# Kernel tuning notes

Measured on AMD Instinct MI355X. Metric: run time of the kernel, lower is better.

## Reference

```python
import jax, jax.numpy as jnp
import numpy as np

B, S, D, H = 2, 2048, 1024, 16
DK = D // H
NEG = -1e9


def setup_inputs() -> dict:
    key = jax.random.key(0)
    ks = jax.random.split(key, 12)
    inp = {
        "query": jax.random.normal(ks[0], (B, S, D), jnp.float32),
        "key": jax.random.normal(ks[1], (B, S, D), jnp.float32),
        "value": jax.random.normal(ks[2], (B, S, D), jnp.float32),
        "mask": jax.random.randint(ks[3], (B, S), 0, 2, jnp.int32),
    }
    # 4 linears (q, k, v, out), each d_model x d_model with bias.
    scale = 1.0 / np.sqrt(D)
    for i, name in enumerate(["wq", "wk", "wv", "wo"]):
        inp[name] = jax.random.uniform(ks[4 + i], (D, D), jnp.float32, -scale, scale)
        inp["b" + name[1]] = jax.random.uniform(ks[8 + i], (D,), jnp.float32, -scale, scale)
    return inp


def _split_heads(x):  # [B,S,D] -> [B,H,S,DK]
    return x.reshape(B, S, H, DK).transpose(0, 2, 1, 3)


def reference(query, key, value, mask, wq, bq, wk, bk, wv, bv, wo, bo):
    q = _split_heads(query @ wq.T + bq)
    k = _split_heads(key @ wk.T + bk)
    v = _split_heads(value @ wv.T + bv)
    scores = jnp.einsum("bhqd,bhkd->bhqk", q, k) / jnp.sqrt(jnp.float32(DK))
    # mask: [B,S] -> [B,1,1,S]; masked_fill where mask == 0
    m = mask[:, None, None, :]
    scores = jnp.where(m == 0, NEG, scores)
    attn = jax.nn.softmax(scores, axis=-1)  # dropout p=0 (eval) -> identity
    x = jnp.einsum("bhqk,bhkd->bhqd", attn, v)
    x = x.transpose(0, 2, 1, 3).reshape(B, S, D)
    return x @ wo.T + bo
```

## Files before the change

kernel.cpp:

```cpp
#include <hip/hip_runtime.h>


typedef _Float16 f16;
typedef _Float16 f16x8 __attribute__((ext_vector_type(8)));
typedef _Float16 f16x4 __attribute__((ext_vector_type(4)));
typedef __fp16 fp16x2r __attribute__((ext_vector_type(2)));
typedef float f32x4 __attribute__((ext_vector_type(4)));

#define MFMA_F16(a, b, c) __builtin_amdgcn_mfma_f32_16x16x32_f16((a), (b), (c), 0, 0, 0)
#define L2E 1.44269504088896340736f

__device__ __forceinline__ void gld16(const void* g, void* l) {
    __builtin_amdgcn_global_load_lds(
        (__attribute__((address_space(1))) void*)(g),
        (__attribute__((address_space(3))) void*)(l), 16, 0, 0);
}

__global__ __launch_bounds__(256) void cvt_kernel(
    const float* __restrict__ q, const float* __restrict__ k,
    const float* __restrict__ v,
    const float* __restrict__ wq, const float* __restrict__ wk,
    const float* __restrict__ wv, const float* __restrict__ wo,
    f16* __restrict__ oq, f16* __restrict__ ok, f16* __restrict__ ov,
    f16* __restrict__ owq, f16* __restrict__ owk, f16* __restrict__ owv,
    f16* __restrict__ owo)
{
    const int z = blockIdx.y;
    const float* src;
    f16* dst;
    int n;
    switch (z) {
        case 0: src = q;  dst = oq;  n = 4194304; break;
        case 1: src = k;  dst = ok;  n = 4194304; break;
        case 2: src = v;  dst = ov;  n = 4194304; break;
        case 3: src = wq; dst = owq; n = 1048576; break;
        case 4: src = wk; dst = owk; n = 1048576; break;
        case 5: src = wv; dst = owv; n = 1048576; break;
        default: src = wo; dst = owo; n = 1048576; break;
    }
    int idx = (blockIdx.x * 256 + threadIdx.x) * 8;
    if (idx >= n) return;
    float4 a = *(const float4*)(src + idx);
    float4 b = *(const float4*)(src + idx + 4);
    f16x8 h = { (f16)a.x, (f16)a.y, (f16)a.z, (f16)a.w,
                (f16)b.x, (f16)b.y, (f16)b.z, (f16)b.w };
    *(f16x8*)(dst + idx) = h;
}

__global__ __launch_bounds__(256) void proj_qkv_kernel(
    const f16* __restrict__ xq, const f16* __restrict__ xk,
    const f16* __restrict__ xv,
    const f16* __restrict__ wqh, const f16* __restrict__ wkh,
    const f16* __restrict__ wvh,
    const float* __restrict__ bq, const float* __restrict__ bk,
    const float* __restrict__ bv,
    f16* __restrict__ qh, f16* __restrict__ kh, f16* __restrict__ vt)
{
    const int z = blockIdx.z;
    const f16* X = (z == 0) ? xq : (z == 1) ? xk : xv;
    const f16* W = (z == 0) ? wqh : (z == 1) ? wkh : wvh;
    const float* bias = (z == 0) ? bq : (z == 1) ? bk : bv;
    const f16* P0 = (z < 2) ? W : X;
    const f16* P1 = (z < 2) ? X : W;

    __shared__ __align__(16) f16 smem[16384];
    f16* As = smem;
    f16* Bs = smem + 8192;
    f16* L  = smem;

    const int t = threadIdx.x;
    const int wave = t >> 6, lane = t & 63, quad = lane >> 4, l15 = lane & 15;
    const int m_base = (wave >> 1) * 64, n_base = (wave & 1) * 64;
    const int blockM = (z < 2) ? blockIdx.y * 128 : blockIdx.x * 128;
    const int blockN = (z < 2) ? blockIdx.x * 128 : blockIdx.y * 128;

    const int srow = lane >> 3;
    const int sblk = (lane & 7) ^ srow;

    f32x4 acc[4][4];
#pragma unroll
    for (int mt = 0; mt < 4; mt++)
#pragma unroll
        for (int nt = 0; nt < 4; nt++)
            acc[mt][nt] = (f32x4){0.f, 0.f, 0.f, 0.f};

    for (int k0 = 0; k0 < 1024; k0 += 64) {
        __syncthreads();
#pragma unroll
        for (int j = 0; j < 4; j++) {
            int r0 = wave * 32 + j * 8;
            gld16(&P0[(size_t)(blockM + r0 + srow) * 1024 + k0 + sblk * 8],
                  &As[r0 * 64]);
            gld16(&P1[(size_t)(blockN + r0 + srow) * 1024 + k0 + sblk * 8],
                  &Bs[r0 * 64]);
        }
        __syncthreads();

#pragma unroll
        for (int c = 0; c < 2; c++) {
            f16x8 af[4], bf[4];
#pragma unroll
            for (int mt = 0; mt < 4; mt++)
                af[mt] = *(const f16x8*)(&As[(m_base + mt * 16 + l15) * 64 +
                                             (((c * 4 + quad) ^ (l15 & 7)) << 3)]);
#pragma unroll
            for (int nt = 0; nt < 4; nt++)
                bf[nt] = *(const f16x8*)(&Bs[(n_base + nt * 16 + l15) * 64 +
                                             (((c * 4 + quad) ^ (l15 & 7)) << 3)]);
#pragma unroll
            for (int mt = 0; mt < 4; mt++)
#pragma unroll
                for (int nt = 0; nt < 4; nt++)
                    acc[mt][nt] = MFMA_F16(af[mt], bf[nt], acc[mt][nt]);
        }
    }

    if (z < 2) {
        f16* o = (z == 0) ? qh : kh;
        const float scale = (z == 0) ? 0.125f * L2E : 1.0f;
        float4 b4[4];
#pragma unroll
        for (int mt = 0; mt < 4; mt++)
            b4[mt] = *(const float4*)(&bias[blockM + m_base + mt * 16 + quad * 4]);

#pragma unroll
        for (int half = 0; half < 2; half++) {
            __syncthreads();
            if ((wave & 1) == half) {
#pragma unroll
                for (int mt = 0; mt < 4; mt++)
#pragma unroll
                    for (int nt = 0; nt < 4; nt++) {
                        f16x4 pk = {
                            (f16)((acc[mt][nt][0] + b4[mt].x) * scale),
                            (f16)((acc[mt][nt][1] + b4[mt].y) * scale),
                            (f16)((acc[mt][nt][2] + b4[mt].z) * scale),
                            (f16)((acc[mt][nt][3] + b4[mt].w) * scale) };
                        *(f16x4*)(&L[(nt * 16 + l15) * 136 +
                                     m_base + mt * 16 + quad * 4]) = pk;
                    }
            }
            __syncthreads();
#pragma unroll
            for (int pass = 0; pass < 4; pass++) {
                int unit = pass * 32 + (t >> 3);
                int hh = unit >> 6, s_loc = unit & 63;
                f16x8 vv = *(const f16x8*)(&L[s_loc * 136 + hh * 64 + (t & 7) * 8]);
                int s_glob = blockN + half * 64 + s_loc;
                int b = s_glob >> 11, s = s_glob & 2047;
                int h_glob = (blockM >> 6) + hh;
                *(f16x8*)(&o[(((size_t)(b * 16 + h_glob) * 2048 + s) << 6) +
                             (t & 7) * 8]) = vv;
            }
        }
    } else {
        float bv_[4];
#pragma unroll
        for (int nt = 0; nt < 4; nt++)
            bv_[nt] = bias[blockN + n_base + nt * 16 + l15];

#pragma unroll
        for (int half = 0; half < 2; half++) {
            __syncthreads();
            if ((wave & 1) == half) {
#pragma unroll
                for (int mt = 0; mt < 4; mt++)
#pragma unroll
                    for (int nt = 0; nt < 4; nt++) {
                        f16x4 pk = { (f16)(acc[mt][nt][0] + bv_[nt]),
                                     (f16)(acc[mt][nt][1] + bv_[nt]),
                                     (f16)(acc[mt][nt][2] + bv_[nt]),
                                     (f16)(acc[mt][nt][3] + bv_[nt]) };
                        *(f16x4*)(&L[(nt * 16 + l15) * 136 +
                                     m_base + mt * 16 + quad * 4]) = pk;
                    }
            }
            __syncthreads();
#pragma unroll
            for (int pass = 0; pass < 4; pass++) {
                int f_loc = pass * 16 + (t >> 4);
                int tt = t & 15;
                int bb = (tt >= 8) ? 64 : 0;
                int o  = (tt & 7) * 8;
                int p  = (o >> 5) & 1;
                int c  = (o >> 3) & 3;
                int g1 = bb + p * 32 + c * 4;
                const f16* Lrow = &L[f_loc * 136];
                f16x4 lo = *(const f16x4*)(&Lrow[g1]);
                f16x4 hi = *(const f16x4*)(&Lrow[g1 + 16]);
                f16x8 vv = __builtin_shufflevector(lo, hi, 0, 1, 2, 3, 4, 5, 6, 7);
                int feat = blockN + half * 64 + f_loc;
                int hh = feat >> 6, dk = feat & 63;
                int b = blockM >> 11;
                int s0 = (blockM & 2047) + bb + o;
                *(f16x8*)(&vt[((size_t)((b * 16 + hh) * 64 + dk) << 11) + s0]) = vv;
            }
        }
    }
}

__device__ __forceinline__ void flash_stage2(
    const f16* kbase, const f16* vbase, int key0,
    f16* Kb, f16* Vb, int wg, int srow8, int sblk)
{
#pragma unroll
    for (int p = 0; p < 2; p++) {
        int r0 = wg * 16 + p * 8;
        int row = r0 + srow8;
        gld16(&kbase[(size_t)(key0 + row) * 64 + sblk * 8], &Kb[r0 * 64]);
        gld16(&vbase[(size_t)row * 2048 + key0 + sblk * 8], &Vb[r0 * 64]);
    }
}

__device__ __forceinline__ void flash_phase2(
    const f16* Kbuf, const f16* Vbuf, const float* bias_all, int key0,
    const f16x8 (&qf)[2][2], int quad, int l15,
    f32x4 (&O)[2][4], f32x4 (&lacc)[2])
{
    const int sw = l15 & 7;
    f32x4 sc[2][4];
#pragma unroll
    for (int nt = 0; nt < 4; nt++) {
        const f16* krow = &Kbuf[(nt * 16 + l15) * 64];
        f16x8 kf0 = *(const f16x8*)(&krow[(quad ^ sw) << 3]);
        f16x8 kf1 = *(const f16x8*)(&krow[((quad + 4) ^ sw) << 3]);
        float4 b4 = *(const float4*)(&bias_all[key0 + nt * 16 + quad * 4]);
#pragma unroll
        for (int cb = 0; cb < 2; cb++) {
            f32x4 z4 = (f32x4){b4.x, b4.y, b4.z, b4.w};
            z4 = MFMA_F16(kf0, qf[cb][0], z4);
            sc[cb][nt] = MFMA_F16(kf1, qf[cb][1], z4);
        }
    }
    const f16x8 ones8 = {(f16)1.f, (f16)1.f, (f16)1.f, (f16)1.f,
                         (f16)1.f, (f16)1.f, (f16)1.f, (f16)1.f};
    union P8u { f16x8 v8; fp16x2r h[4]; };
    P8u pp[2][2];
#pragma unroll
    for (int cb = 0; cb < 2; cb++) {
#pragma unroll
        for (int nt = 0; nt < 4; nt++) {
            float p0 = __builtin_amdgcn_exp2f(sc[cb][nt][0]);
            float p1 = __builtin_amdgcn_exp2f(sc[cb][nt][1]);
            float p2 = __builtin_amdgcn_exp2f(sc[cb][nt][2]);
            float p3 = __builtin_amdgcn_exp2f(sc[cb][nt][3]);
            pp[cb][nt >> 1].h[(nt & 1) * 2 + 0] = __builtin_amdgcn_cvt_pkrtz(p0, p1);
            pp[cb][nt >> 1].h[(nt & 1) * 2 + 1] = __builtin_amdgcn_cvt_pkrtz(p2, p3);
        }
        lacc[cb] = MFMA_F16(ones8, pp[cb][0].v8, lacc[cb]);
        lacc[cb] = MFMA_F16(ones8, pp[cb][1].v8, lacc[cb]);
    }
#pragma unroll
    for (int nto = 0; nto < 4; nto++) {
        const f16* vrow = &Vbuf[(nto * 16 + l15) * 64];
        f16x8 va = *(const f16x8*)(&vrow[(quad ^ sw) << 3]);
        f16x8 vb = *(const f16x8*)(&vrow[((4 + quad) ^ sw) << 3]);
#pragma unroll
        for (int cb = 0; cb < 2; cb++) {
            O[cb][nto] = MFMA_F16(va, pp[cb][0].v8, O[cb][nto]);
            O[cb][nto] = MFMA_F16(vb, pp[cb][1].v8, O[cb][nto]);
        }
    }
}

__global__
__attribute__((amdgpu_flat_work_group_size(512, 512)))
__attribute__((amdgpu_waves_per_eu(4, 4)))
void flash_kernel(
    const f16* __restrict__ qh, const f16* __restrict__ kh,
    const f16* __restrict__ vt, const int* __restrict__ mask,
    f16* __restrict__ ctx)
{
    __shared__ __align__(16) f16 KV[8 * 4096];
    __shared__ float bias_all[2048];

    const int t = threadIdx.x;
    const int wave = t >> 6, lane = t & 63, quad = lane >> 4, l15 = lane & 15;
    const int group = wave >> 2, wg = wave & 3;
    const int bh = blockIdx.x;
    const int b = bh >> 4, h = bh & 15;
    const int q0 = blockIdx.y * 128;

    const f16* qbase = qh + (size_t)bh * (2048 * 64);
    const f16* kbase = kh + (size_t)bh * (2048 * 64);
    const f16* vbase = vt + (size_t)bh * (64 * 2048);

    f16* K0 = &KV[((0 * 2 + group) * 2 + 0) * 4096];
    f16* V0 = &KV[((0 * 2 + group) * 2 + 1) * 4096];
    f16* K1 = &KV[((1 * 2 + group) * 2 + 0) * 4096];
    f16* V1 = &KV[((1 * 2 + group) * 2 + 1) * 4096];

#pragma unroll
    for (int j = 0; j < 4; j++) {
        int i = j * 512 + t;
        bias_all[i] = (mask[b * 2048 + i] == 0) ? -1.0e9f : 0.0f;
    }

    f16x8 qf[2][2];
#pragma unroll
    for (int cb = 0; cb < 2; cb++) {
        int qrow = q0 + wg * 32 + cb * 16 + l15;
        qf[cb][0] = *(const f16x8*)(&qbase[qrow * 64 + quad * 8]);
        qf[cb][1] = *(const f16x8*)(&qbase[qrow * 64 + 32 + quad * 8]);
    }

    f32x4 O[2][4];
#pragma unroll
    for (int cb = 0; cb < 2; cb++)
#pragma unroll
        for (int n = 0; n < 4; n++) O[cb][n] = (f32x4){0.f, 0.f, 0.f, 0.f};
    f32x4 lacc[2] = {(f32x4){0.f, 0.f, 0.f, 0.f}, (f32x4){0.f, 0.f, 0.f, 0.f}};

    const int srow8 = lane >> 3;
    const int sblk = (lane & 7) ^ srow8;

    flash_stage2(kbase, vbase, group * 64, K0, V0, wg, srow8, sblk);

    for (int k2 = 0; k2 < 16; k2 += 2) {
        __syncthreads();
        flash_stage2(kbase, vbase, (k2 + 1) * 128 + group * 64, K1, V1,
                     wg, srow8, sblk);
        flash_phase2(K0, V0, bias_all, k2 * 128 + group * 64,
                     qf, quad, l15, O, lacc);
        __syncthreads();
        if (k2 < 14)
            flash_stage2(kbase, vbase, (k2 + 2) * 128 + group * 64, K0, V0,
                         wg, srow8, sblk);
        flash_phase2(K1, V1, bias_all, (k2 + 1) * 128 + group * 64,
                     qf, quad, l15, O, lacc);
    }

    __syncthreads();
    float* Red = (float*)KV;
    const int t4 = wg * 64 + lane;
    if (group == 1) {
#pragma unroll
        for (int cb = 0; cb < 2; cb++) {
#pragma unroll
            for (int nto = 0; nto < 4; nto++)
                *(f32x4*)(&Red[(cb * 4 + nto) * 1024 + t4 * 4]) = O[cb][nto];
            Red[8 * 1024 + cb * 256 + t4] = lacc[cb][0];
        }
    }
    __syncthreads();
    if (group == 0) {
#pragma unroll
        for (int cb = 0; cb < 2; cb++) {
            const float l2 = Red[8 * 1024 + cb * 256 + t4];
            const float inv_l = 1.0f / (lacc[cb][0] + l2);
            int qrow = q0 + wg * 32 + cb * 16 + l15;
#pragma unroll
            for (int nto = 0; nto < 4; nto++) {
                f32x4 o2 = *(const f32x4*)(&Red[(cb * 4 + nto) * 1024 + t4 * 4]);
                f16x4 pk = { (f16)((O[cb][nto][0] + o2[0]) * inv_l),
                             (f16)((O[cb][nto][1] + o2[1]) * inv_l),
                             (f16)((O[cb][nto][2] + o2[2]) * inv_l),
                             (f16)((O[cb][nto][3] + o2[3]) * inv_l) };
                *(f16x4*)(&ctx[(size_t)(b * 2048 + qrow) * 1024 + h * 64 +
                               nto * 16 + quad * 4]) = pk;
            }
        }
    }
}

__global__ __launch_bounds__(256) void proj_out_kernel(
    const f16* __restrict__ ctx, const f16* __restrict__ woh,
    const float* __restrict__ bo, float* __restrict__ out)
{
    __shared__ __align__(16) f16 As[2][128 * 64];
    __shared__ __align__(16) f16 Bs[2][64 * 64];

    const int t = threadIdx.x;
    const int wave = t >> 6, lane = t & 63, quad = lane >> 4, l15 = lane & 15;
    const int m_base = (wave >> 1) * 64, n_base = (wave & 1) * 32;
    const int blockM = blockIdx.x * 128;
    const int blockN = blockIdx.y * 64;

    const int srow = lane >> 3;
    const int sblk = (lane & 7) ^ srow;

    f32x4 acc[4][2];
#pragma unroll
    for (int mt = 0; mt < 4; mt++)
#pragma unroll
        for (int nt = 0; nt < 2; nt++)
            acc[mt][nt] = (f32x4){0.f, 0.f, 0.f, 0.f};

#pragma unroll
    for (int j = 0; j < 4; j++) {
        int r0 = wave * 32 + j * 8;
        gld16(&ctx[(size_t)(blockM + r0 + srow) * 1024 + sblk * 8],
              &As[0][r0 * 64]);
    }
#pragma unroll
    for (int j = 0; j < 2; j++) {
        int r0 = wave * 16 + j * 8;
        gld16(&woh[(size_t)(blockN + r0 + srow) * 1024 + sblk * 8],
              &Bs[0][r0 * 64]);
    }

    for (int ki = 0; ki < 16; ki++) {
        const int cur = ki & 1;
        __syncthreads();

        if (ki < 15) {
            const int k0n = (ki + 1) * 64;
#pragma unroll
            for (int j = 0; j < 4; j++) {
                int r0 = wave * 32 + j * 8;
                gld16(&ctx[(size_t)(blockM + r0 + srow) * 1024 + k0n + sblk * 8],
                      &As[cur ^ 1][r0 * 64]);
            }
#pragma unroll
            for (int j = 0; j < 2; j++) {
                int r0 = wave * 16 + j * 8;
                gld16(&woh[(size_t)(blockN + r0 + srow) * 1024 + k0n + sblk * 8],
                      &Bs[cur ^ 1][r0 * 64]);
            }
        }

#pragma unroll
        for (int c = 0; c < 2; c++) {
            f16x8 af[4], bf[2];
#pragma unroll
            for (int mt = 0; mt < 4; mt++)
                af[mt] = *(const f16x8*)(&As[cur][(m_base + mt * 16 + l15) * 64 +
                                              (((c * 4 + quad) ^ (l15 & 7)) << 3)]);
#pragma unroll
            for (int nt = 0; nt < 2; nt++)
                bf[nt] = *(const f16x8*)(&Bs[cur][(n_base + nt * 16 + l15) * 64 +
                                              (((c * 4 + quad) ^ (l15 & 7)) << 3)]);
#pragma unroll
            for (int mt = 0; mt < 4; mt++)
#pragma unroll
                for (int nt = 0; nt < 2; nt++)
                    acc[mt][nt] = MFMA_F16(af[mt], bf[nt], acc[mt][nt]);
        }
    }

    float bo_[2];
#pragma unroll
    for (int nt = 0; nt < 2; nt++)
        bo_[nt] = bo[blockN + n_base + nt * 16 + l15];

#pragma unroll
    for (int mt = 0; mt < 4; mt++) {
        int row0 = blockM + m_base + mt * 16 + quad * 4;
#pragma unroll
        for (int nt = 0; nt < 2; nt++) {
            int col_g = blockN + n_base + nt * 16 + l15;
#pragma unroll
            for (int i = 0; i < 4; i++)
                out[(size_t)(row0 + i) * 1024 + col_g] = acc[mt][nt][i] + bo_[nt];
        }
    }
}

extern "C" void kernel_launch(void* const* d_in, const int* in_sizes, int n_in,
                              void* d_out, int out_size, void* d_ws, size_t ws_size,
                              hipStream_t stream) {
    const float* query = (const float*)d_in[0];
    const float* key_  = (const float*)d_in[1];
    const float* value = (const float*)d_in[2];
    const int*   mask  = (const int*)d_in[3];
    const float* wq = (const float*)d_in[4];
    const float* bq = (const float*)d_in[5];
    const float* wk = (const float*)d_in[6];
    const float* bk = (const float*)d_in[7];
    const float* wv = (const float*)d_in[8];
    const float* bv = (const float*)d_in[9];
    const float* wo = (const float*)d_in[10];
    const float* bo = (const float*)d_in[11];
    float* out = (float*)d_out;

    f16* xq  = (f16*)d_ws;
    f16* xk  = xq  + 4194304;
    f16* xv  = xk  + 4194304;
    f16* wqh = xv  + 4194304;
    f16* wkh = wqh + 1048576;
    f16* wvh = wkh + 1048576;
    f16* woh = wvh + 1048576;
    f16* qh  = woh + 1048576;
    f16* kh  = qh  + 4194304;
    f16* vt  = kh  + 4194304;
    f16* ctx = xq;

    cvt_kernel<<<dim3(2048, 7), 256, 0, stream>>>(
        query, key_, value, wq, wk, wv, wo, xq, xk, xv, wqh, wkh, wvh, woh);
    proj_qkv_kernel<<<dim3(32, 8, 3), 256, 0, stream>>>(
        xq, xk, xv, wqh, wkh, wvh, bq, bk, bv, qh, kh, vt);
    flash_kernel<<<dim3(32, 16), 512, 0, stream>>>(qh, kh, vt, mask, ctx);
    proj_out_kernel<<<dim3(32, 16), 256, 0, stream>>>(ctx, woh, bo, out);
}
```

Baseline: 212.7 us.

## Triple-buffer projection GEMMs with K=32 stages and explicit vmcnt waits

Both the QKV projection and output projection GEMMs move from single/double-buffered K=64 tiles to a three-stage ring of K=32 tiles. Each stage is loaded directly into LDS with global_load_lds, and the loop waits through manual s_waitcnt vmcnt counts plus raw s_barrier, so loads for two steps ahead overlap MFMA work. The LDS XOR swizzle is reworked for 32-wide rows. This raises LDS use and depends on hand-counted outstanding-load accounting, which could race if the counts are wrong.

New measurement: 209.2 us. No clear change (-1.6%).

```diff
diff --git a/kernel.cpp b/kernel.cpp
--- a/kernel.cpp
+++ b/kernel.cpp
@@ -47,6 +47,21 @@
     *(f16x8*)(dst + idx) = h;
 }
 
+__device__ __forceinline__ void stage_qkv(
+    const f16* __restrict__ P0, const f16* __restrict__ P1,
+    int blockM, int blockN, int k0, f16* Ad, f16* Bd,
+    int wave, int srow2, int schunk)
+{
+#pragma unroll
+    for (int p = 0; p < 2; p++) {
+        int r0 = wave * 32 + p * 16;
+        gld16(&P0[(size_t)(blockM + r0 + srow2) * 1024 + k0 + schunk * 8],
+              &Ad[r0 * 32]);
+        gld16(&P1[(size_t)(blockN + r0 + srow2) * 1024 + k0 + schunk * 8],
+              &Bd[r0 * 32]);
+    }
+}
+
 __global__ __launch_bounds__(256) void proj_qkv_kernel(
     const f16* __restrict__ xq, const f16* __restrict__ xk,
     const f16* __restrict__ xv,
@@ -63,10 +78,8 @@
     const f16* P0 = (z < 2) ? W : X;
     const f16* P1 = (z < 2) ? X : W;
 
-    __shared__ __align__(16) f16 smem[16384];
-    f16* As = smem;
-    f16* Bs = smem + 8192;
-    f16* L  = smem;
+    __shared__ __align__(16) f16 smem[24576];
+    f16* L = smem;
 
     const int t = threadIdx.x;
     const int wave = t >> 6, lane = t & 63, quad = lane >> 4, l15 = lane & 15;
@@ -74,8 +87,8 @@
     const int blockM = (z < 2) ? blockIdx.y * 128 : blockIdx.x * 128;
     const int blockN = (z < 2) ? blockIdx.x * 128 : blockIdx.y * 128;
 
-    const int srow = lane >> 3;
-    const int sblk = (lane & 7) ^ srow;
+    const int srow2 = lane >> 2;
+    const int schunk = (lane & 3) ^ (srow2 & 3);
 
     f32x4 acc[4][4];
 #pragma unroll
@@ -84,35 +97,41 @@
         for (int nt = 0; nt < 4; nt++)
             acc[mt][nt] = (f32x4){0.f, 0.f, 0.f, 0.f};
 
-    for (int k0 = 0; k0 < 1024; k0 += 64) {
-        __syncthreads();
-#pragma unroll
-        for (int j = 0; j < 4; j++) {
-            int r0 = wave * 32 + j * 8;
-            gld16(&P0[(size_t)(blockM + r0 + srow) * 1024 + k0 + sblk * 8],
-                  &As[r0 * 64]);
-            gld16(&P1[(size_t)(blockN + r0 + srow) * 1024 + k0 + sblk * 8],
-                  &Bs[r0 * 64]);
-        }
-        __syncthreads();
-
-#pragma unroll
-        for (int c = 0; c < 2; c++) {
-            f16x8 af[4], bf[4];
-#pragma unroll
-            for (int mt = 0; mt < 4; mt++)
-                af[mt] = *(const f16x8*)(&As[(m_base + mt * 16 + l15) * 64 +
-                                             (((c * 4 + quad) ^ (l15 & 7)) << 3)]);
+    f16 *Ac = smem,          *An = smem + 4096,  *Af = smem + 8192;
+    f16 *Bc = smem + 12288,  *Bn = smem + 16384, *Bf = smem + 20480;
+
+    stage_qkv(P0, P1, blockM, blockN, 0,  Ac, Bc, wave, srow2, schunk);
+    stage_qkv(P0, P1, blockM, blockN, 32, An, Bn, wave, srow2, schunk);
+    asm volatile("s_waitcnt vmcnt(4)" ::: "memory");
+
+    for (int ki = 0; ki < 32; ki++) {
+        __builtin_amdgcn_s_barrier();
+        __builtin_amdgcn_sched_barrier(0);
+        if (ki < 30)
+            stage_qkv(P0, P1, blockM, blockN, (ki + 2) * 32, Af, Bf,
+                      wave, srow2, schunk);
+
+        f16x8 af[4], bf[4];
+#pragma unroll
+        for (int mt = 0; mt < 4; mt++)
+            af[mt] = *(const f16x8*)(&Ac[(m_base + mt * 16 + l15) * 32 +
+                                         ((quad ^ (l15 & 3)) << 3)]);
+#pragma unroll
+        for (int nt = 0; nt < 4; nt++)
+            bf[nt] = *(const f16x8*)(&Bc[(n_base + nt * 16 + l15) * 32 +
+                                         ((quad ^ (l15 & 3)) << 3)]);
+#pragma unroll
+        for (int mt = 0; mt < 4; mt++)
 #pragma unroll
             for (int nt = 0; nt < 4; nt++)
-                bf[nt] = *(const f16x8*)(&Bs[(n_base + nt * 16 + l15) * 64 +
-                                             (((c * 4 + quad) ^ (l15 & 7)) << 3)]);
-#pragma unroll
-            for (int mt = 0; mt < 4; mt++)
-#pragma unroll
-                for (int nt = 0; nt < 4; nt++)
-                    acc[mt][nt] = MFMA_F16(af[mt], bf[nt], acc[mt][nt]);
-        }
+                acc[mt][nt] = MFMA_F16(af[mt], bf[nt], acc[mt][nt]);
+
+        if (ki < 30)
+            asm volatile("s_waitcnt vmcnt(4)" ::: "memory");
+        else if (ki == 30)
+            asm volatile("s_waitcnt vmcnt(0)" ::: "memory");
+        f16* tA = Ac; Ac = An; An = Af; Af = tA;
+        f16* tB = Bc; Bc = Bn; Bn = Bf; Bf = tB;
     }
 
     if (z < 2) {
@@ -363,12 +382,29 @@
     }
 }
 
+__device__ __forceinline__ void stage_out(
+    const f16* __restrict__ ctx, const f16* __restrict__ woh,
+    int blockM, int blockN, int k0, f16* Ad, f16* Bd,
+    int wave, int srow2, int schunk)
+{
+#pragma unroll
+    for (int p = 0; p < 2; p++) {
+        int r0 = wave * 32 + p * 16;
+        gld16(&ctx[(size_t)(blockM + r0 + srow2) * 1024 + k0 + schunk * 8],
+              &Ad[r0 * 32]);
+    }
+    {
+        int r0 = wave * 16;
+        gld16(&woh[(size_t)(blockN + r0 + srow2) * 1024 + k0 + schunk * 8],
+              &Bd[r0 * 32]);
+    }
+}
+
 __global__ __launch_bounds__(256) void proj_out_kernel(
     const f16* __restrict__ ctx, const f16* __restrict__ woh,
     const float* __restrict__ bo, float* __restrict__ out)
 {
-    __shared__ __align__(16) f16 As[2][128 * 64];
-    __shared__ __align__(16) f16 Bs[2][64 * 64];
+    __shared__ __align__(16) f16 smem[18432];
 
     const int t = threadIdx.x;
     const int wave = t >> 6, lane = t & 63, quad = lane >> 4, l15 = lane & 15;
@@ -376,8 +412,8 @@
     const int blockM = blockIdx.x * 128;
     const int blockN = blockIdx.y * 64;
 
-    const int srow = lane >> 3;
-    const int sblk = (lane & 7) ^ srow;
+    const int srow2 = lane >> 2;
+    const int schunk = (lane & 3) ^ (srow2 & 3);
 
     f32x4 acc[4][2];
 #pragma unroll
@@ -386,56 +422,41 @@
         for (int nt = 0; nt < 2; nt++)
             acc[mt][nt] = (f32x4){0.f, 0.f, 0.f, 0.f};
 
-#pragma unroll
-    for (int j = 0; j < 4; j++) {
-        int r0 = wave * 32 + j * 8;
-        gld16(&ctx[(size_t)(blockM + r0 + srow) * 1024 + sblk * 8],
-              &As[0][r0 * 64]);
-    }
-#pragma unroll
-    for (int j = 0; j < 2; j++) {
-        int r0 = wave * 16 + j * 8;
-        gld16(&woh[(size_t)(blockN + r0 + srow) * 1024 + sblk * 8],
-              &Bs[0][r0 * 64]);
-    }
-
-    for (int ki = 0; ki < 16; ki++) {
-        const int cur = ki & 1;
-        __syncthreads();
-
-        if (ki < 15) {
-            const int k0n = (ki + 1) * 64;
-#pragma unroll
-            for (int j = 0; j < 4; j++) {
-                int r0 = wave * 32 + j * 8;
-                gld16(&ctx[(size_t)(blockM + r0 + srow) * 1024 + k0n + sblk * 8],
-                      &As[cur ^ 1][r0 * 64]);
-            }
-#pragma unroll
-            for (int j = 0; j < 2; j++) {
-                int r0 = wave * 16 + j * 8;
-                gld16(&woh[(size_t)(blockN + r0 + srow) * 1024 + k0n + sblk * 8],
-                      &Bs[cur ^ 1][r0 * 64]);
-            }
-        }
-
-#pragma unroll
-        for (int c = 0; c < 2; c++) {
-            f16x8 af[4], bf[2];
-#pragma unroll
-            for (int mt = 0; mt < 4; mt++)
-                af[mt] = *(const f16x8*)(&As[cur][(m_base + mt * 16 + l15) * 64 +
-                                              (((c * 4 + quad) ^ (l15 & 7)) << 3)]);
+    f16 *Ac = smem,          *An = smem + 4096,  *Af = smem + 8192;
+    f16 *Bc = smem + 12288,  *Bn = smem + 14336, *Bf = smem + 16384;
+
+    stage_out(ctx, woh, blockM, blockN, 0,  Ac, Bc, wave, srow2, schunk);
+    stage_out(ctx, woh, blockM, blockN, 32, An, Bn, wave, srow2, schunk);
+    asm volatile("s_waitcnt vmcnt(3)" ::: "memory");
+
+    for (int ki = 0; ki < 32; ki++) {
+        __builtin_amdgcn_s_barrier();
+        __builtin_amdgcn_sched_barrier(0);
+        if (ki < 30)
+            stage_out(ctx, woh, blockM, blockN, (ki + 2) * 32, Af, Bf,
+                      wave, srow2, schunk);
+
+        f16x8 af[4], bf[2];
+#pragma unroll
+        for (int mt = 0; mt < 4; mt++)
+            af[mt] = *(const f16x8*)(&Ac[(m_base + mt * 16 + l15) * 32 +
+                                         ((quad ^ (l15 & 3)) << 3)]);
+#pragma unroll
+        for (int nt = 0; nt < 2; nt++)
+            bf[nt] = *(const f16x8*)(&Bc[(n_base + nt * 16 + l15) * 32 +
+                                         ((quad ^ (l15 & 3)) << 3)]);
+#pragma unroll
+        for (int mt = 0; mt < 4; mt++)
 #pragma unroll
             for (int nt = 0; nt < 2; nt++)
-                bf[nt] = *(const f16x8*)(&Bs[cur][(n_base + nt * 16 + l15) * 64 +
-                                              (((c * 4 + quad) ^ (l15 & 7)) << 3)]);
-#pragma unroll
-            for (int mt = 0; mt < 4; mt++)
-#pragma unroll
-                for (int nt = 0; nt < 2; nt++)
-                    acc[mt][nt] = MFMA_F16(af[mt], bf[nt], acc[mt][nt]);
-        }
+                acc[mt][nt] = MFMA_F16(af[mt], bf[nt], acc[mt][nt]);
+
+        if (ki < 30)
+            asm volatile("s_waitcnt vmcnt(3)" ::: "memory");
+        else if (ki == 30)
+            asm volatile("s_waitcnt vmcnt(0)" ::: "memory");
+        f16* tA = Ac; Ac = An; An = Af; Af = tA;
+        f16* tB = Bc; Bc = Bn; Bn = Bf; Bf = tB;
     }
 
     float bo_[2];
```
